# Performance work log

Measured on AMD Instinct MI355X. Metric: run time of the kernel, lower is better.

## Reference

```python
import jax, jax.numpy as jnp
import numpy as np

DIM = 192
HEADS = 6
B = 4
H = 64
W = 64
L = H * W  # kv length must equal h*w for the torch 'else' repeat branch
TOPK = 4
N_EXPERTS = 12
PADS = [0, 1, 2] * 4
GROUPS = [1] * 6 + [DIM] * 6


def conv2d(x, w, b=None, pad=0, groups=1):
    out = jax.lax.conv_general_dilated(
        x, w, (1, 1), [(pad, pad), (pad, pad)],
        dimension_numbers=("NCHW", "OIHW", "NCHW"),
        feature_group_count=groups)
    if b is not None:
        out = out + b[None, :, None, None]
    return out


def l2norm(x):
    # torch F.normalize(dim=-1): x / max(||x||_2, 1e-12)
    return x / jnp.maximum(jnp.linalg.norm(x, axis=-1, keepdims=True), 1e-12)


def attention_ca(I, T, proj_w):
    b, c, h, w = I.shape
    l = T.shape[2]
    # F.avg_pool1d(kv.transpose(1,2), 4) pools the CHANNEL dim, kernel=stride=4
    pooled = T.transpose(0, 2, 1).reshape(b, l, c // 4, 4).mean(-1)  # [b, l, c/4]
    x_pool = pooled.transpose(0, 2, 1)  # [b, c/4, l]
    q = l2norm(I.reshape(b, HEADS, c // HEADS, h * w))
    k = l2norm(x_pool.reshape(b, HEADS, c // (4 * HEADS), l))
    v = k  # v = normalize(x_pool) = k
    # h == 64 -> torch 'else' branch: repeat(1, 1, 4, 1) on channel dim
    k = jnp.tile(k, (1, 1, 4, 1))
    v = jnp.tile(v, (1, 1, 4, 1))
    attn = jax.nn.softmax(jnp.einsum("bhcl,bhdl->bhcd", q, k), axis=-1)
    out = jnp.einsum("bhcd,bhdl->bhcl", attn, v).reshape(b, c, h, w)
    return conv2d(out, proj_w)


def ex_forward(x, fmap, ex_ws, ex_bs, out_w, out_b):
    # AdaptiveAvgPool3d((1,1,12)) applied to a 4D tensor [b,c,h,w]:
    # full mean over dims 1 (c) and 2 (h), adaptive 12-bin pooling over dim 3 (w)
    m = fmap.mean(axis=(1, 2))  # [b, w]
    win = m.shape[-1]
    bins = [m[:, (i * win) // 12: -(-((i + 1) * win) // 12)].mean(-1) for i in range(12)]
    wvec = jax.nn.softmax(jnp.stack(bins, axis=-1), axis=-1)  # [b, 12]
    _, idx = jax.lax.top_k(wvec[0], TOPK)  # module uses batch element 0 only
    branches = [
        (lambda xx, j=j: conv2d(xx, ex_ws[j], ex_bs[j], pad=PADS[j], groups=GROUPS[j]))
        for j in range(N_EXPERTS)
    ]
    outs = [jax.lax.switch(idx[i], branches, x) for i in range(TOPK)]
    return conv2d(jnp.concatenate(outs, axis=1), out_w, out_b, pad=1)


def forward(I, T, temperature, ca1_proj_w, ex_ws, ex_bs, ex_out_w, ex_out_b,
            kv_w, kv_dw_w, q_dw_w, proj_w):
    b, c, h, w = I.shape
    fmap = attention_ca(I, T, ca1_proj_w)
    fmap = ex_forward(I, fmap, ex_ws, ex_bs, ex_out_w, ex_out_b)
    kv = conv2d(conv2d(fmap, kv_w), kv_dw_w, pad=1, groups=2 * c)
    k, v = jnp.split(kv, 2, axis=1)
    q = conv2d(fmap, q_dw_w, pad=1, groups=c)
    q = l2norm(q.reshape(b, HEADS, c // HEADS, h * w))
    k = l2norm(k.reshape(b, HEADS, c // HEADS, h * w))
    v = v.reshape(b, HEADS, c // HEADS, h * w)
    attn = jax.nn.softmax(jnp.einsum("bhcl,bhdl->bhcd", q, k) * temperature[None], axis=-1)
    out = jnp.einsum("bhcd,bhdl->bhcl", attn, v).reshape(b, c, h, w)
    return conv2d(out, proj_w)


def setup_inputs() -> dict:
    key = jax.random.key(0)
    ks = jax.random.split(key, 64)
    def rn(i, shape, s=0.05):
        return jax.random.normal(ks[i], shape, dtype=jnp.float32) * s
    d = DIM
    inp = {
        "I": rn(0, (B, d, H, W), 1.0),
        "T": rn(1, (B, d, L), 1.0),
        "temperature": jnp.ones((HEADS, 1, 1), dtype=jnp.float32),
        "ca1_proj_w": rn(2, (d, d, 1, 1)),
        "ex_out_w": rn(3, (d, 4 * d, 3, 3), 0.02),
        "ex_out_b": rn(4, (d,), 0.01),
        "kv_w": rn(5, (2 * d, d, 1, 1)),
        "kv_dw_w": rn(6, (2 * d, 1, 3, 3)),
        "q_dw_w": rn(7, (d, 1, 3, 3)),
        "proj_w": rn(8, (d, d, 1, 1)),
    }
    ksz = [1, 3, 5] * 4
    for j in range(N_EXPERTS):
        cin = d if j < 6 else 1
        inp[f"ex_w{j}"] = rn(10 + j, (d, cin, ksz[j], ksz[j]), 0.05)
        inp[f"ex_b{j}"] = rn(30 + j, (d,), 0.01)
    return inp


def reference(I, T, temperature, ca1_proj_w,
              ex_w0, ex_w1, ex_w2, ex_w3, ex_w4, ex_w5,
              ex_w6, ex_w7, ex_w8, ex_w9, ex_w10, ex_w11,
              ex_b0, ex_b1, ex_b2, ex_b3, ex_b4, ex_b5,
              ex_b6, ex_b7, ex_b8, ex_b9, ex_b10, ex_b11,
              ex_out_w, ex_out_b, kv_w, kv_dw_w, q_dw_w, proj_w):
    ex_ws = [ex_w0, ex_w1, ex_w2, ex_w3, ex_w4, ex_w5,
             ex_w6, ex_w7, ex_w8, ex_w9, ex_w10, ex_w11]
    ex_bs = [ex_b0, ex_b1, ex_b2, ex_b3, ex_b4, ex_b5,
             ex_b6, ex_b7, ex_b8, ex_b9, ex_b10, ex_b11]
    return forward(I, T, temperature, ca1_proj_w, ex_ws, ex_bs,
                   ex_out_w, ex_out_b, kv_w, kv_dw_w, q_dw_w, proj_w)
```

## Files before the change

### kernel.cpp

```cpp
#include <hip/hip_runtime.h>
#include <math.h>


struct ExPtrs { const float* w[12]; const float* b[12]; };
struct BfPtrs { const short* adt[6]; const float* bias[6]; };

typedef __attribute__((ext_vector_type(8))) short short8v;
typedef __attribute__((ext_vector_type(4))) short short4v;
typedef __attribute__((ext_vector_type(4))) float f32x4;

__device__ __forceinline__ void fma4(float4& a, float s, const float4& v) {
    a.x = fmaf(s, v.x, a.x); a.y = fmaf(s, v.y, a.y);
    a.z = fmaf(s, v.z, a.z); a.w = fmaf(s, v.w, a.w);
}

__device__ __forceinline__ short f2bf(float v) {
    unsigned u = __float_as_uint(v);
    return (short)((u + 0x7FFFu + ((u >> 16) & 1u)) >> 16);
}

__global__ void zero_kernel(float* __restrict__ p, int n) {
    for (int i = blockIdx.x * 256 + threadIdx.x; i < n; i += gridDim.x * 256) p[i] = 0.f;
}

__global__ void packIbf_kernel(const float* __restrict__ I, short* __restrict__ Ibf) {
    const int n = 4 * 68 * 68 * 192;
    for (int o = blockIdx.x * 256 + threadIdx.x; o < n; o += gridDim.x * 256) {
        int ch = o % 192;
        int t = o / 192;
        int xx = t % 68; t /= 68;
        int yy = t % 68;
        int b = t / 68;
        short v = 0;
        if (yy >= 2 && yy < 66 && xx >= 2 && xx < 66)
            v = f2bf(I[(((size_t)(b * 192 + ch)) << 12) + (yy - 2) * 64 + (xx - 2)]);
        Ibf[o] = v;
    }
}

__global__ void packAd_kernel(const float* __restrict__ w, short* __restrict__ Ad, int K2) {
    int n = K2 * 12 * 6 * 64 * 8;
    for (int o = blockIdx.x * 256 + threadIdx.x; o < n; o += gridDim.x * 256) {
        int u = o & 7;
        int t = o >> 3;
        int l = t & 63; t >>= 6;
        int ksg = t % 6; t /= 6;
        int mt = t % 12;
        int tap = t / 12;
        int oc = mt * 16 + (l & 15);
        int ic = ksg * 32 + (l >> 4) * 8 + u;
        Ad[o] = f2bf(w[(((size_t)oc * 192) + ic) * K2 + tap]);
    }
}

__global__ void packA_kernel(const float* __restrict__ exow, short* __restrict__ At) {
    const int n = 9 * 12 * 24 * 64 * 8;
    for (int o = blockIdx.x * 256 + threadIdx.x; o < n; o += gridDim.x * 256) {
        int j = o & 7;
        int t = o >> 3;
        int l = t & 63; t >>= 6;
        int ksg = t % 24; t /= 24;
        int mt = t % 12;
        int tap = t / 12;
        int oc = mt * 16 + (l & 15);
        int icg = ksg * 32 + (l >> 4) * 8 + j;
        At[o] = f2bf(exow[((size_t)oc * 768 + icg) * 9 + tap]);
    }
}

__global__ void wtr8_kernel(const float* __restrict__ w, float* __restrict__ wt,
                            int OCg, int IC, int K2) {
    int n = OCg * IC * K2 * 8;
    for (int o = blockIdx.x * 256 + threadIdx.x; o < n; o += gridDim.x * 256) {
        int u = o & 7;
        int t = o >> 3;
        int kk = t % K2;
        int t2 = t / K2;
        int ic = t2 % IC;
        int og = t2 / IC;
        wt[o] = w[(((size_t)(og * 8 + u)) * IC + ic) * K2 + kk];
    }
}


__global__ void pool64_kernel(const float* __restrict__ T, double* __restrict__ xp) {
    int j = blockIdx.x;
    for (int l = threadIdx.x; l < 4096; l += 256) {
        const float* t = T + ((size_t)(4 * j)) * 4096 + l;
        double s = (double)t[0] + (double)t[4096] + (double)t[2 * 4096] + (double)t[3 * 4096];
        xp[(size_t)j * 4096 + l] = 0.25 * s;
    }
}

__global__ void norm64_f32_kernel(const float* __restrict__ src, double* __restrict__ dst) {
    size_t off = (size_t)blockIdx.x * 4096;
    double acc = 0.0;
    for (int i = threadIdx.x; i < 4096; i += 256) { double v = src[off + i]; acc += v * v; }
    __shared__ double red[256];
    red[threadIdx.x] = acc; __syncthreads();
    for (int st = 128; st > 0; st >>= 1) {
        if (threadIdx.x < st) red[threadIdx.x] += red[threadIdx.x + st];
        __syncthreads();
    }
    double scale = 1.0 / fmax(sqrt(red[0]), 1e-12);
    for (int i = threadIdx.x; i < 4096; i += 256) dst[off + i] = src[off + i] * scale;
}

__global__ void norm64_f64_kernel(double* __restrict__ buf) {
    size_t off = (size_t)blockIdx.x * 4096;
    double acc = 0.0;
    for (int i = threadIdx.x; i < 4096; i += 256) { double v = buf[off + i]; acc += v * v; }
    __shared__ double red[256];
    red[threadIdx.x] = acc; __syncthreads();
    for (int st = 128; st > 0; st >>= 1) {
        if (threadIdx.x < st) red[threadIdx.x] += red[threadIdx.x + st];
        __syncthreads();
    }
    double scale = 1.0 / fmax(sqrt(red[0]), 1e-12);
    for (int i = threadIdx.x; i < 4096; i += 256) buf[off + i] *= scale;
}

__global__ void attnA64p_kernel(const double* __restrict__ qn, const double* __restrict__ kn,
                                double* __restrict__ PA) {
    int hh = blockIdx.x, cc = blockIdx.y;
    int t = threadIdx.x;
    int c = t >> 3, d = t & 7;
    const double* q = qn + ((size_t)(hh * 32 + c)) * 4096 + cc * 256;
    const double* k = kn + ((size_t)(hh * 8 + d)) * 4096 + cc * 256;
    double acc = 0.0;
    for (int i = 0; i < 256; ++i) acc += q[i] * k[i];
    PA[((size_t)((hh * 32 + c) * 8 + d)) * 16 + cc] = acc;
}

__global__ void attnA64r_kernel(const double* __restrict__ PA, double* __restrict__ A) {
    int hh = blockIdx.x;
    int t = threadIdx.x;
    int c = t >> 3, d = t & 7;
    double acc = 0.0;
    const double* p = PA + ((size_t)((hh * 32 + c) * 8 + d)) * 16;
    for (int cc = 0; cc < 16; ++cc) acc += p[cc];
    __shared__ double S[32][8];
    S[c][d] = acc;
    __syncthreads();
    if (t < 32) {
        double mx = -1e300;
        for (int j = 0; j < 8; ++j) mx = fmax(mx, S[t][j]);
        double e[8], sum = 0.0;
        for (int j = 0; j < 8; ++j) { e[j] = exp(S[t][j] - mx); sum += e[j]; }
        double inv = 1.0 / sum;
        for (int j = 0; j < 8; ++j) A[((size_t)(hh * 32 + t)) * 8 + j] = e[j] * inv;
    }
}

__global__ void aout64_kernel(const double* __restrict__ A, const double* __restrict__ kn,
                              double* __restrict__ out) {
    int l = blockIdx.x * 256 + threadIdx.x;
    int ch = blockIdx.y;
    int hh = ch >> 5;
    const double* a = A + (size_t)ch * 8;
    const double* v = kn + ((size_t)(hh * 8)) * 4096 + l;
    double acc = 0.0;
    #pragma unroll
    for (int d = 0; d < 8; ++d) acc += a[d] * v[(size_t)d * 4096];
    out[(size_t)ch * 4096 + l] = acc;
}

__global__ void fm64_kernel(const double* __restrict__ in, const float* __restrict__ w,
                            double* __restrict__ out) {
    int l = blockIdx.x * 256 + threadIdx.x;
    int oc = blockIdx.y;
    const double* src = in + l;
    const float* wr = w + (size_t)oc * 192;
    double acc = 0.0;
    for (int ic = 0; ic < 192; ++ic) acc += (double)wr[ic] * src[(size_t)ic * 4096];
    out[(size_t)oc * 4096 + l] = acc;
}

__global__ void meanx64_kernel(const double* __restrict__ fm, double* __restrict__ m) {
    int x = blockIdx.x;
    double acc = 0.0;
    for (int t = threadIdx.x; t < 192 * 64; t += 256) {
        int c = t >> 6, y = t & 63;
        acc += fm[(size_t)c * 4096 + y * 64 + x];
    }
    __shared__ double red[256];
    red[threadIdx.x] = acc; __syncthreads();
    for (int st = 128; st > 0; st >>= 1) {
        if (threadIdx.x < st) red[threadIdx.x] += red[threadIdx.x + st];
        __syncthreads();
    }
    if (threadIdx.x == 0) m[x] = red[0] / (192.0 * 64.0);
}

__global__ void route64_kernel(const double* __restrict__ m, int* __restrict__ idx) {
    if (threadIdx.x != 0) return;
    double bins[12];
    for (int i = 0; i < 12; ++i) {
        int st = (i * 64) / 12;
        int en = ((i + 1) * 64 + 11) / 12;
        double s = 0.0;
        for (int j = st; j < en; ++j) s += m[j];
        bins[i] = s / (double)(en - st);
    }
    bool used[12] = {};
    for (int s = 0; s < 4; ++s) {
        int best = 0; double bv = -1e300;
        for (int j = 0; j < 12; ++j)
            if (!used[j] && bins[j] > bv) { best = j; bv = bins[j]; }
        used[best] = true;
        idx[s] = best;
    }
}


__global__ void rownorm_kernel(const float* __restrict__ src, float* __restrict__ dst) {
    size_t off = (size_t)blockIdx.x * 4096;
    const float* s = src + off;
    float acc = 0.f;
    for (int i = threadIdx.x; i < 4096; i += 256) { float v = s[i]; acc += v * v; }
    __shared__ float red[256];
    red[threadIdx.x] = acc; __syncthreads();
    for (int st = 128; st > 0; st >>= 1) {
        if (threadIdx.x < st) red[threadIdx.x] += red[threadIdx.x + st];
        __syncthreads();
    }
    float scale = 1.0f / fmaxf(sqrtf(red[0]), 1e-12f);
    float* d = dst + off;
    for (int i = threadIdx.x; i < 4096; i += 256) d[i] = s[i] * scale;
}

template<int KK>
__device__ __forceinline__ void dmf_body(const short* __restrict__ Ad,
                                         const short* __restrict__ Ibf,
                                         const float* __restrict__ bias,
                                         short* __restrict__ Ebf, int cslot,
                                         int b, int y, short* __restrict__ sb) {
    constexpr int P = (KK - 1) / 2;
    int tid = threadIdx.x;
    int lane = tid & 63, wave = tid >> 6;
    int mt = blockIdx.y * 4 + wave;
    int ln = lane & 15, kb = lane >> 4;
    f32x4 acc[4];
    #pragma unroll
    for (int c = 0; c < 4; ++c)
        #pragma unroll
        for (int r = 0; r < 4; ++r)
            acc[c][r] = bias[mt * 16 + kb * 4 + r];
    for (int r = 0; r < KK; ++r) {
        const short* src = Ibf + ((size_t)(b * 68 + y + 2 - P + r)) * 68 * 192;
        if (r > 0) __syncthreads();
        for (int g2 = tid; g2 < 68 * 24; g2 += 256) {
            int px = g2 / 24, ck = g2 % 24;
            *(short8v*)(sb + px * 200 + ck * 8) = *(const short8v*)(src + px * 192 + ck * 8);
        }
        __syncthreads();
        for (int dx = 0; dx < KK; ++dx) {
            int tap = r * KK + dx;
            const short* Ab = Ad + (((size_t)(tap * 12 + mt)) * 6 * 64 + lane) * 8;
            #pragma unroll
            for (int ks = 0; ks < 6; ++ks) {
                short8v av = *(const short8v*)(Ab + ks * 512);
                int kc = ks * 32 + kb * 8;
                #pragma unroll
                for (int c = 0; c < 4; ++c) {
                    short8v bv = *(const short8v*)(sb + ((2 - P) + dx + c * 16 + ln) * 200 + kc);
                    acc[c] = __builtin_amdgcn_mfma_f32_16x16x32_bf16(av, bv, acc[c], 0, 0, 0);
                }
            }
        }
    }
    #pragma unroll
    for (int c = 0; c < 4; ++c) {
        int x = c * 16 + ln;
        short* d = Ebf + (((size_t)(b * 66 + y + 1)) * 68 + (x + 1)) * 384 + cslot * 192 + mt * 16 + kb * 4;
        short4v o;
        #pragma unroll
        for (int r = 0; r < 4; ++r) o[r] = f2bf(acc[c][r]);
        *(short4v*)d = o;
    }
}

__global__ void dense_mfma_kernel(BfPtrs bp, const short* __restrict__ Ibf,
                                  const int* __restrict__ idx, int slot,
                                  short* __restrict__ Ebf, int cslot) {
    __shared__ short sb[68 * 200];
    int j = idx[slot];
    j = j < 0 ? 0 : (j > 11 ? 11 : j);
    if (j >= 6) return;
    int y = blockIdx.x, b = blockIdx.z;
    int m = j % 3;
    if (m == 0) dmf_body<1>(bp.adt[j], Ibf, bp.bias[j], Ebf, cslot, b, y, sb);
    else if (m == 1) dmf_body<3>(bp.adt[j], Ibf, bp.bias[j], Ebf, cslot, b, y, sb);
    else dmf_body<5>(bp.adt[j], Ibf, bp.bias[j], Ebf, cslot, b, y, sb);
}

__global__ void dw_bf_kernel(const float* __restrict__ I, ExPtrs ep,
                             const int* __restrict__ idx, int slot,
                             short* __restrict__ Ebf, int cslot) {
    int j = idx[slot];
    j = j < 0 ? 0 : (j > 11 ? 11 : j);
    if (j < 6) return;
    int K = 1 + 2 * (j % 3), pad = j % 3;
    const float* w = ep.w[j];
    const float* bias = ep.b[j];
    int l = blockIdx.x * 256 + threadIdx.x;
    int ch = blockIdx.y, b = blockIdx.z;
    int y = l >> 6, x = l & 63;
    float acc = bias[ch];
    const float* src = I + ((size_t)(b * 192 + ch)) * 4096;
    for (int ky = 0; ky < K; ++ky)
        for (int kx = 0; kx < K; ++kx) {
            int yy = y + ky - pad, xx = x + kx - pad;
            if (yy >= 0 && yy < 64 && xx >= 0 && xx < 64)
                acc += w[((size_t)ch * K + ky) * K + kx] * src[yy * 64 + xx];
        }
    Ebf[(((size_t)(b * 66 + y + 1)) * 68 + (x + 1)) * 384 + cslot * 192 + ch] = f2bf(acc);
}

__global__ void exout_mfma_kernel(const short* __restrict__ At, const short* __restrict__ Ebf,
                                  const float* __restrict__ bias, float* __restrict__ out,
                                  int pass) {
    __shared__ short sb[68 * 392];
    int y = blockIdx.x, b = blockIdx.z;
    int tid = threadIdx.x;
    int lane = tid & 63, wave = tid >> 6;
    int mt = blockIdx.y * 4 + wave;
    int ln = lane & 15, kb = lane >> 4;
    float* dst = out + ((size_t)(b * 192 + mt * 16)) * 4096 + y * 64;
    f32x4 acc[4];
    if (pass == 0) {
        #pragma unroll
        for (int c = 0; c < 4; ++c)
            #pragma unroll
            for (int r = 0; r < 4; ++r)
                acc[c][r] = bias[mt * 16 + kb * 4 + r];
    } else {
        #pragma unroll
        for (int c = 0; c < 4; ++c)
            #pragma unroll
            for (int r = 0; r < 4; ++r)
                acc[c][r] = dst[(size_t)(kb * 4 + r) * 4096 + c * 16 + ln];
    }
    for (int r = 0; r < 3; ++r) {
        const short* src = Ebf + ((size_t)(b * 66 + y + r)) * 68 * 384;
        if (r > 0) __syncthreads();
        for (int g2 = tid; g2 < 68 * 48; g2 += 256) {
            int px = g2 / 48, ck = g2 % 48;
            *(short8v*)(sb + px * 392 + ck * 8) = *(const short8v*)(src + px * 384 + ck * 8);
        }
        __syncthreads();
        for (int dx = 0; dx < 3; ++dx) {
            int tap = r * 3 + dx;
            const short* Ab = At + (((size_t)((tap * 12 + mt) * 24) + pass * 12) * 64 + lane) * 8;
            #pragma unroll
            for (int ks = 0; ks < 12; ++ks) {
                short8v av = *(const short8v*)(Ab + (size_t)ks * 512);
                int kc = ks * 32 + kb * 8;
                #pragma unroll
                for (int c = 0; c < 4; ++c) {
                    short8v bv = *(const short8v*)(sb + (dx + c * 16 + ln) * 392 + kc);
                    acc[c] = __builtin_amdgcn_mfma_f32_16x16x32_bf16(av, bv, acc[c], 0, 0, 0);
                }
            }
        }
    }
    #pragma unroll
    for (int c = 0; c < 4; ++c)
        #pragma unroll
        for (int r = 0; r < 4; ++r)
            dst[(size_t)(kb * 4 + r) * 4096 + c * 16 + ln] = acc[c][r];
}

__global__ void conv1x1_sw_kernel(const float* __restrict__ in, const float* __restrict__ wtg,
                                  float* __restrict__ out) {
    int tid = threadIdx.x;
    int xq = tid & 15, ry = tid >> 4;
    int tile = blockIdx.x, og = blockIdx.y, b = blockIdx.z;
    int p0 = tile * 1024 + ry * 64 + xq * 4;
    float4 acc[8] = {};
    const float* src = in + (size_t)b * 192 * 4096 + p0;
    const float* wp = wtg + (size_t)og * 192 * 8;
    for (int ic = 0; ic < 192; ic += 2) {
        float4 xv0 = *(const float4*)(src + (size_t)ic * 4096);
        float4 xv1 = *(const float4*)(src + (size_t)(ic + 1) * 4096);
        float4 wA0 = *(const float4*)(wp + ic * 8);
        float4 wB0 = *(const float4*)(wp + ic * 8 + 4);
        float4 wA1 = *(const float4*)(wp + ic * 8 + 8);
        float4 wB1 = *(const float4*)(wp + ic * 8 + 12);
        fma4(acc[0], wA0.x, xv0); fma4(acc[1], wA0.y, xv0);
        fma4(acc[2], wA0.z, xv0); fma4(acc[3], wA0.w, xv0);
        fma4(acc[4], wB0.x, xv0); fma4(acc[5], wB0.y, xv0);
        fma4(acc[6], wB0.z, xv0); fma4(acc[7], wB0.w, xv0);
        fma4(acc[0], wA1.x, xv1); fma4(acc[1], wA1.y, xv1);
        fma4(acc[2], wA1.z, xv1); fma4(acc[3], wA1.w, xv1);
        fma4(acc[4], wB1.x, xv1); fma4(acc[5], wB1.y, xv1);
        fma4(acc[6], wB1.z, xv1); fma4(acc[7], wB1.w, xv1);
    }
    float* dst = out + ((size_t)(b * 192 + og * 8)) * 4096 + p0;
    #pragma unroll
    for (int u = 0; u < 8; ++u)
        *(float4*)(dst + (size_t)u * 4096) = acc[u];
}

__global__ void dwconv_kernel(const float* __restrict__ in, const float* __restrict__ w,
                              float* __restrict__ out) {
    int l = blockIdx.x * 256 + threadIdx.x;
    int ch = blockIdx.y, b = blockIdx.z;
    int y = l >> 6, x = l & 63;
    const float* src = in + ((size_t)(b * 192 + ch)) * 4096;
    const float* wk = w + ch * 9;
    float acc = 0.f;
    #pragma unroll
    for (int ky = 0; ky < 3; ++ky)
        #pragma unroll
        for (int kx = 0; kx < 3; ++kx) {
            int yy = y + ky - 1, xx = x + kx - 1;
            if (yy >= 0 && yy < 64 && xx >= 0 && xx < 64)
                acc += wk[ky * 3 + kx] * src[yy * 64 + xx];
        }
    out[((size_t)(b * 192 + ch)) * 4096 + l] = acc;
}

__global__ void attnF_row_kernel(const float* __restrict__ qn, const float* __restrict__ kn,
                                 const float* __restrict__ temp, float* __restrict__ AF) {
    int row = blockIdx.x;
    int hh = (row >> 5) % 6, b = row / 192;
    int tid = threadIdx.x;
    const float* q = qn + ((size_t)(b * 192) + (row % 192)) * 4096;
    const float* kb = kn + ((size_t)(b * 192 + hh * 32)) * 4096;
    float acc[32];
    #pragma unroll
    for (int d = 0; d < 32; ++d) acc[d] = 0.f;
    for (int i = tid; i < 4096; i += 256) {
        float qv = q[i];
        #pragma unroll
        for (int d = 0; d < 32; ++d) acc[d] += qv * kb[(size_t)d * 4096 + i];
    }
    #pragma unroll
    for (int d = 0; d < 32; ++d) {
        acc[d] += __shfl_xor(acc[d], 32);
        acc[d] += __shfl_xor(acc[d], 16);
        acc[d] += __shfl_xor(acc[d], 8);
        acc[d] += __shfl_xor(acc[d], 4);
        acc[d] += __shfl_xor(acc[d], 2);
        acc[d] += __shfl_xor(acc[d], 1);
    }
    __shared__ float red[4][32];
    int wid = tid >> 6, lane = tid & 63;
    if (lane == 0) {
        #pragma unroll
        for (int d = 0; d < 32; ++d) red[wid][d] = acc[d];
    }
    __syncthreads();
    if (tid < 32) {
        float s = red[0][tid] + red[1][tid] + red[2][tid] + red[3][tid];
        s *= temp[hh];
        float mx = s;
        mx = fmaxf(mx, __shfl_xor(mx, 16));
        mx = fmaxf(mx, __shfl_xor(mx, 8));
        mx = fmaxf(mx, __shfl_xor(mx, 4));
        mx = fmaxf(mx, __shfl_xor(mx, 2));
        mx = fmaxf(mx, __shfl_xor(mx, 1));
        float e = expf(s - mx);
        float sum = e;
        sum += __shfl_xor(sum, 16);
        sum += __shfl_xor(sum, 8);
        sum += __shfl_xor(sum, 4);
        sum += __shfl_xor(sum, 2);
        sum += __shfl_xor(sum, 1);
        AF[(size_t)row * 32 + tid] = e / sum;
    }
}

__global__ void attnF_out_kernel(const float* __restrict__ AF, const float* __restrict__ v,
                                 float* __restrict__ out) {
    int l = blockIdx.x * 256 + threadIdx.x;
    int ch = blockIdx.y, b = blockIdx.z;
    int hh = ch >> 5, c = ch & 31;
    const float* a = AF + ((size_t)((b * 6 + hh) * 32 + c)) * 32;
    const float* vp = v + ((size_t)(b * 192 + hh * 32)) * 4096 + l;
    float acc = 0.f;
    #pragma unroll
    for (int d = 0; d < 32; ++d) acc += a[d] * vp[(size_t)d * 4096];
    out[((size_t)(b * 192 + ch)) * 4096 + l] = acc;
}

extern "C" void kernel_launch(void* const* d_in, const int* in_sizes, int n_in,
                              void* d_out, int out_size, void* d_ws, size_t ws_size,
                              hipStream_t stream) {
    const float* I    = (const float*)d_in[0];
    const float* T    = (const float*)d_in[1];
    const float* temp = (const float*)d_in[2];
    const float* ca1  = (const float*)d_in[3];
    const float* exow = (const float*)d_in[4];
    const float* exob = (const float*)d_in[5];
    const float* kvw  = (const float*)d_in[6];
    const float* kvdw = (const float*)d_in[7];
    const float* qdw  = (const float*)d_in[8];
    const float* projw= (const float*)d_in[9];
    ExPtrs ep;
    for (int j = 0; j < 12; ++j) {
        ep.w[j] = (const float*)d_in[10 + 2 * j];
        ep.b[j] = (const float*)d_in[11 + 2 * j];
    }

    float* ws   = (float*)d_ws;
    float* AF   = ws;
    int*   idxb = (int*)(ws + 24576);
    float* R0   = ws + 32768;
    float* R1   = R0 + 3145728;
    float* IbfF = R1 + 3145728;
    float* EbfF = IbfF + 3551232;
    double* dsm = (double*)(EbfF + 3446784);
    double* A64 = dsm;
    double* m64 = dsm + 1536;
    double* PA  = dsm + 1600;
    float* wtkv   = (float*)(dsm + 26176);
    float* wtproj = wtkv + 73728;
    short* At     = (short*)(wtproj + 36864);
    short* Adt    = At + 1327104;
    size_t adtoff[6] = {0, 36864, 368640, 1290240, 1327104, 1658880};
    double* xpool64 = (double*)R0;
    double* qn64    = (double*)(R0 + 393216);
    double* aout64  = (double*)R1;
    double* fm64    = (double*)(R1 + 1572864);
    short* Ibf = (short*)IbfF;
    short* Ebf = (short*)EbfF;
    float* KN = IbfF;
    float* V  = EbfF;
    BfPtrs bp;
    for (int j = 0; j < 6; ++j) { bp.adt[j] = Adt + adtoff[j]; bp.bias[j] = ep.b[j]; }
    float* out  = (float*)d_out;

    dim3 g(16, 192, 4), gs8(4, 24, 4), gmf(64, 3, 4);

    for (int j = 0; j < 6; ++j) {
        int KK = 1 + 2 * (j % 3);
        packAd_kernel<<<512, 256, 0, stream>>>(ep.w[j], Adt + adtoff[j], KK * KK);
    }
    packA_kernel<<<1024, 256, 0, stream>>>(exow, At);
    wtr8_kernel<<<256, 256, 0, stream>>>(kvw, wtkv, 48, 192, 1);
    wtr8_kernel<<<256, 256, 0, stream>>>(projw, wtproj, 24, 192, 1);
    packIbf_kernel<<<2048, 256, 0, stream>>>(I, Ibf);

    pool64_kernel<<<48, 256, 0, stream>>>(T, xpool64);
    norm64_f32_kernel<<<192, 256, 0, stream>>>(I, qn64);
    norm64_f64_kernel<<<48, 256, 0, stream>>>(xpool64);
    attnA64p_kernel<<<dim3(6, 16), 256, 0, stream>>>(qn64, xpool64, PA);
    attnA64r_kernel<<<6, 256, 0, stream>>>(PA, A64);
    aout64_kernel<<<dim3(16, 192), 256, 0, stream>>>(A64, xpool64, aout64);
    fm64_kernel<<<dim3(16, 192), 256, 0, stream>>>(aout64, ca1, fm64);
    meanx64_kernel<<<64, 256, 0, stream>>>(fm64, m64);
    route64_kernel<<<1, 64, 0, stream>>>(m64, idxb);

    zero_kernel<<<2048, 256, 0, stream>>>(EbfF, 3446784);
    for (int s = 0; s < 4; ++s) {
        dense_mfma_kernel<<<gmf, 256, 0, stream>>>(bp, Ibf, idxb, s, Ebf, s & 1);
        dw_bf_kernel<<<g, 256, 0, stream>>>(I, ep, idxb, s, Ebf, s & 1);
        if (s == 1) {
            exout_mfma_kernel<<<gmf, 256, 0, stream>>>(At, Ebf, exob, R1, 0);
            zero_kernel<<<2048, 256, 0, stream>>>(EbfF, 3446784);
        }
        if (s == 3)
            exout_mfma_kernel<<<gmf, 256, 0, stream>>>(At, Ebf, exob, R1, 1);
    }

    conv1x1_sw_kernel<<<gs8, 256, 0, stream>>>(R1, wtkv, R0);
    dwconv_kernel<<<g, 256, 0, stream>>>(R0, kvdw, KN);
    rownorm_kernel<<<768, 256, 0, stream>>>(KN, KN);
    dwconv_kernel<<<g, 256, 0, stream>>>(R1, qdw, R0);
    rownorm_kernel<<<768, 256, 0, stream>>>(R0, R0);
    attnF_row_kernel<<<768, 256, 0, stream>>>(R0, KN, temp, AF);
    conv1x1_sw_kernel<<<gs8, 256, 0, stream>>>(R1, wtkv + 36864, R0);
    dwconv_kernel<<<g, 256, 0, stream>>>(R0, kvdw + 192 * 9, V);

    attnF_out_kernel<<<g, 256, 0, stream>>>(AF, V, R0);
    conv1x1_sw_kernel<<<gs8, 256, 0, stream>>>(R0, wtproj, out);
}
```

Baseline: 622.9 us.

## Compute routing mean algebraically instead of materializing attention output and projection

```diff
diff --git a/kernel.cpp b/kernel.cpp
--- a/kernel.cpp
+++ b/kernel.cpp
@@ -152,44 +152,36 @@
     }
 }
 
-__global__ void aout64_kernel(const double* __restrict__ A, const double* __restrict__ kn,
-                              double* __restrict__ out) {
-    int l = blockIdx.x * 256 + threadIdx.x;
-    int ch = blockIdx.y;
-    int hh = ch >> 5;
-    const double* a = A + (size_t)ch * 8;
-    const double* v = kn + ((size_t)(hh * 8)) * 4096 + l;
-    double acc = 0.0;
-    #pragma unroll
-    for (int d = 0; d < 8; ++d) acc += a[d] * v[(size_t)d * 4096];
-    out[(size_t)ch * 4096 + l] = acc;
-}
-
-__global__ void fm64_kernel(const double* __restrict__ in, const float* __restrict__ w,
-                            double* __restrict__ out) {
-    int l = blockIdx.x * 256 + threadIdx.x;
-    int oc = blockIdx.y;
-    const double* src = in + l;
-    const float* wr = w + (size_t)oc * 192;
-    double acc = 0.0;
-    for (int ic = 0; ic < 192; ++ic) acc += (double)wr[ic] * src[(size_t)ic * 4096];
-    out[(size_t)oc * 4096 + l] = acc;
-}
-
-__global__ void meanx64_kernel(const double* __restrict__ fm, double* __restrict__ m) {
-    int x = blockIdx.x;
-    double acc = 0.0;
-    for (int t = threadIdx.x; t < 192 * 64; t += 256) {
-        int c = t >> 6, y = t & 63;
-        acc += fm[(size_t)c * 4096 + y * 64 + x];
-    }
-    __shared__ double red[256];
-    red[threadIdx.x] = acc; __syncthreads();
-    for (int st = 128; st > 0; st >>= 1) {
-        if (threadIdx.x < st) red[threadIdx.x] += red[threadIdx.x + st];
-        __syncthreads();
-    }
-    if (threadIdx.x == 0) m[x] = red[0] / (192.0 * 64.0);
+__global__ void kcol64_kernel(const double* __restrict__ kn, double* __restrict__ kcol) {
+    int j = blockIdx.x, x = threadIdx.x;
+    const double* s = kn + (size_t)j * 4096 + x;
+    double acc = 0.0;
+    for (int y = 0; y < 64; ++y) acc += s[y * 64];
+    kcol[j * 64 + x] = acc;
+}
+
+__global__ void wsum64_kernel(const float* __restrict__ ca1, double* __restrict__ wsum) {
+    int ic = threadIdx.x;
+    if (ic >= 192) return;
+    double acc = 0.0;
+    for (int oc = 0; oc < 192; ++oc) acc += (double)ca1[(size_t)oc * 192 + ic];
+    wsum[ic] = acc;
+}
+
+__global__ void mroute64_kernel(const double* __restrict__ A, const double* __restrict__ kcol,
+                                const double* __restrict__ wsum, double* __restrict__ m) {
+    int x = threadIdx.x;
+    if (x >= 64) return;
+    double acc = 0.0;
+    for (int ic = 0; ic < 192; ++ic) {
+        int hh = ic >> 5;
+        double s = 0.0;
+        #pragma unroll
+        for (int d = 0; d < 8; ++d)
+            s += A[(size_t)ic * 8 + d] * kcol[(hh * 8 + d) * 64 + x];
+        acc += wsum[ic] * s;
+    }
+    m[x] = acc / (192.0 * 64.0);
 }
 
 __global__ void route64_kernel(const double* __restrict__ m, int* __restrict__ idx) {
@@ -515,15 +507,15 @@
     double* A64 = dsm;
     double* m64 = dsm + 1536;
     double* PA  = dsm + 1600;
-    float* wtkv   = (float*)(dsm + 26176);
+    double* kcol = dsm + 26176;
+    double* wsum = dsm + 29248;
+    float* wtkv   = (float*)(dsm + 29440);
     float* wtproj = wtkv + 73728;
     short* At     = (short*)(wtproj + 36864);
     short* Adt    = At + 1327104;
     size_t adtoff[6] = {0, 36864, 368640, 1290240, 1327104, 1658880};
     double* xpool64 = (double*)R0;
     double* qn64    = (double*)(R0 + 393216);
-    double* aout64  = (double*)R1;
-    double* fm64    = (double*)(R1 + 1572864);
     short* Ibf = (short*)IbfF;
     short* Ebf = (short*)EbfF;
     float* KN = IbfF;
@@ -548,9 +540,9 @@
     norm64_f64_kernel<<<48, 256, 0, stream>>>(xpool64);
     attnA64p_kernel<<<dim3(6, 16), 256, 0, stream>>>(qn64, xpool64, PA);
     attnA64r_kernel<<<6, 256, 0, stream>>>(PA, A64);
-    aout64_kernel<<<dim3(16, 192), 256, 0, stream>>>(A64, xpool64, aout64);
-    fm64_kernel<<<dim3(16, 192), 256, 0, stream>>>(aout64, ca1, fm64);
-    meanx64_kernel<<<64, 256, 0, stream>>>(fm64, m64);
+    kcol64_kernel<<<48, 64, 0, stream>>>(xpool64, kcol);
+    wsum64_kernel<<<1, 192, 0, stream>>>(ca1, wsum);
+    mroute64_kernel<<<1, 64, 0, stream>>>(A64, kcol, wsum, m64);
     route64_kernel<<<1, 64, 0, stream>>>(m64, idxb);
 
     zero_kernel<<<2048, 256, 0, stream>>>(EbfF, 3446784);
```

After: 569.2 us. 1.09x faster.
